# Kernel optimization log

Hardware: AMD Instinct MI355X
Metric: run time of the kernel (lower is better)

Reference implementation:

```python
import jax, jax.numpy as jnp
import numpy as np

SCALE = 0.1  # literal .mul(0.1) in the source, not 1/sqrt(d_k)


def setup_inputs() -> dict:
    key = jax.random.key(0)
    kq, kk, kv = jax.random.split(key, 3)
    B, S, D, Dv = 8, 2048, 1024, 1024
    q = jax.random.normal(kq, (B, S, D), dtype=jnp.float32)
    k = jax.random.normal(kk, (B, D, S), dtype=jnp.float32)  # note [B, D, S]: matmul(q, k) with no transpose
    v = jax.random.normal(kv, (B, S, Dv), dtype=jnp.float32)
    return {"q": q, "k": k, "v": v}


def reference(q, k, v):
    # s = (q @ k) * 0.1 ; a = softmax(s, -1) ; dropout in eval -> identity ; r = a @ v
    s = jnp.einsum('bsd,bdt->bst', q, k) * SCALE  # [B, S, S]
    a = jax.nn.softmax(s, axis=-1)
    r = jnp.einsum('bst,btv->bsv', a, v)          # [B, S, Dv]
    return r
```

## Files before the change

kernel.cpp:

```cpp
#include <hip/hip_runtime.h>
#include <stdint.h>

#define SEQ 2048
#define DHK 1024
#define DHV 1024
#define NB 8

typedef __attribute__((ext_vector_type(8))) short bf16x8;
typedef __attribute__((ext_vector_type(4))) float f32x4;

__device__ __forceinline__ unsigned short f2bf(float f) {
    uint32_t u = __builtin_bit_cast(uint32_t, f);
    u += 0x7fffu + ((u >> 16) & 1u);
    return (unsigned short)(u >> 16);
}

__device__ __forceinline__ void gload_lds16(const unsigned short* g, unsigned short* l) {
    __builtin_amdgcn_global_load_lds(
        (const __attribute__((address_space(1))) void*)g,
        (__attribute__((address_space(3))) void*)l,
        16, 0, 0);
}

#define WG_BARRIER() asm volatile("s_barrier" ::: "memory")

__global__ __launch_bounds__(256) void fused_cvt(const float* __restrict__ q,
                                                 const float* __restrict__ k,
                                                 const float* __restrict__ v,
                                                 unsigned short* __restrict__ Qb,
                                                 unsigned short* __restrict__ Kt,
                                                 unsigned short* __restrict__ Vt) {
    __shared__ float tile[64][65];
    int bid = blockIdx.x;
    if (bid < 4096) {
        size_t i = ((size_t)bid * 256 + threadIdx.x) * 16;
#pragma unroll
        for (int c = 0; c < 4; ++c) {
            float4 x = *(const float4*)(q + i + c * 4);
            ushort4 o;
            o.x = f2bf(x.x); o.y = f2bf(x.y); o.z = f2bf(x.z); o.w = f2bf(x.w);
            *(ushort4*)(Qb + i + c * 4) = o;
        }
        return;
    }
    const float* in;
    unsigned short* out;
    int R, C, b, x, y;
    if (bid < 8192) {
        int id = bid - 4096;
        b = id >> 9; int rem = id & 511;
        x = rem & 31; y = rem >> 5;
        in = k; out = Kt; R = DHK; C = SEQ;
    } else {
        int id = bid - 8192;
        b = id >> 9; int rem = id & 511;
        x = rem & 15; y = rem >> 4;
        in = v; out = Vt; R = SEQ; C = DHV;
    }
    int c0 = x * 64, r0 = y * 64;
    const float* ib = in + (size_t)b * R * C;
    unsigned short* ob = out + (size_t)b * R * C;
    int tr = threadIdx.x >> 4;
    int tc = (threadIdx.x & 15) * 4;
#pragma unroll
    for (int it = 0; it < 4; ++it) {
        int r = tr + it * 16;
        float4 w = *(const float4*)(ib + (size_t)(r0 + r) * C + c0 + tc);
        tile[r][tc + 0] = w.x; tile[r][tc + 1] = w.y;
        tile[r][tc + 2] = w.z; tile[r][tc + 3] = w.w;
    }
    __syncthreads();
#pragma unroll
    for (int it = 0; it < 4; ++it) {
        int c = tr + it * 16;
        ushort4 o;
        o.x = f2bf(tile[tc + 0][c]);
        o.y = f2bf(tile[tc + 1][c]);
        o.z = f2bf(tile[tc + 2][c]);
        o.w = f2bf(tile[tc + 3][c]);
        *(ushort4*)(ob + (size_t)(c0 + c) * R + r0 + tc) = o;
    }
}

template <int MODE>
__global__ __launch_bounds__(512, 2) void attn_gemm8(const unsigned short* __restrict__ A,
                                                     const unsigned short* __restrict__ Bt,
                                                     void* __restrict__ Cout) {
    constexpr int K   = (MODE == 0) ? DHK : SEQ;
    constexpr int N   = (MODE == 0) ? SEQ : DHV;
    constexpr int TN  = N / 256;
    constexpr int NKT = K / 64;
    constexpr int NITER = NKT / 2;

    __shared__ __attribute__((aligned(16))) unsigned short As[2][256 * 64];
    __shared__ __attribute__((aligned(16))) unsigned short Bs[2][256 * 64];

    const int lid   = blockIdx.x;
    const int batch = lid & 7;
    const int t     = lid >> 3;
    const int bm    = t / TN;
    const int bn    = t % TN;

    const int tid  = threadIdx.x;
    const int wv   = tid >> 6;
    const int lane = tid & 63;
    const int wm   = wv & 1;
    const int wn   = wv >> 1;
    const int m16  = lane & 15;
    const int q    = lane >> 4;
    const int sw   = m16 & 7;
    const int lane_row = lane >> 3;
    const int g    = (lane & 7) ^ lane_row;

    const unsigned short* Ab = A  + (size_t)batch * SEQ * K;
    const unsigned short* Bb = Bt + (size_t)batch * N * K;
    const unsigned short* Ag = Ab + (size_t)(bm * 256 + lane_row) * K + g * 8;
    const unsigned short* Bg = Bb + (size_t)(bn * 256 + lane_row) * K + g * 8;

    auto stage = [&](int ktile, int sub) {
        const int buf = ktile & 1;
        const int k0  = ktile * 64;
#pragma unroll
        for (int c = 0; c < 2; ++c) {
            const int lrow = wv * 16 + c * 8;
            if (sub < 2) {
                const int rb = sub * 128 + lrow;
                gload_lds16(Bg + (size_t)rb * K + k0, &Bs[buf][rb * 64]);
            } else {
                const int rb = (sub == 2 ? 0 : 64) + lrow + (lrow & 64);
                gload_lds16(Ag + (size_t)rb * K + k0, &As[buf][rb * 64]);
            }
        }
    };

    f32x4 acc[8][4];
#pragma unroll
    for (int i = 0; i < 8; ++i)
#pragma unroll
        for (int j = 0; j < 4; ++j)
#pragma unroll
            for (int e = 0; e < 4; ++e) acc[i][j][e] = 0.0f;

    f32x4 acc1[8];
#pragma unroll
    for (int i = 0; i < 8; ++i)
#pragma unroll
        for (int e = 0; e < 4; ++e) acc1[i][e] = 0.0f;
    const short one_bf = (short)0x3F80;
    const bf16x8 ones = {one_bf, one_bf, one_bf, one_bf, one_bf, one_bf, one_bf, one_bf};

#pragma unroll
    for (int ht = 0; ht < 7; ++ht) stage(ht >> 2, ht & 3);
    asm volatile("s_waitcnt vmcnt(6)" ::: "memory");
    WG_BARRIER();

    bf16x8 bfr[4][2];
#pragma unroll 1
    for (int it = 0; it < NITER; ++it) {
        const bool notlast = (it + 1 < NITER);
#pragma unroll
        for (int p = 0; p < 8; ++p) {
            const int qd   = p & 3;
            const int rbuf = p >> 2;
            bf16x8 af[2][2];
#pragma unroll
            for (int i = 0; i < 2; ++i) {
                const int mrow = wm * 128 + (qd * 2 + i) * 16 + m16;
#pragma unroll
                for (int ss = 0; ss < 2; ++ss)
                    af[i][ss] = *(const bf16x8*)&As[rbuf][mrow * 64 + ((ss * 4 + q) ^ sw) * 8];
            }
            if (qd == 0) {
#pragma unroll
                for (int nt = 0; nt < 4; ++nt) {
                    const int nrow = wn * 64 + nt * 16 + m16;
#pragma unroll
                    for (int ss = 0; ss < 2; ++ss)
                        bfr[nt][ss] = *(const bf16x8*)&Bs[rbuf][nrow * 64 + ((ss * 4 + q) ^ sw) * 8];
                }
            }
            if (p == 0 || notlast) stage((7 + it * 8 + p) >> 2, (7 + p) & 3);
            WG_BARRIER();
            __builtin_amdgcn_s_setprio(1);
#pragma unroll
            for (int ss = 0; ss < 2; ++ss)
#pragma unroll
                for (int i = 0; i < 2; ++i) {
                    const int mt = qd * 2 + i;
#pragma unroll
                    for (int nt = 0; nt < 4; ++nt)
                        acc[mt][nt] = __builtin_amdgcn_mfma_f32_16x16x32_bf16(
                            af[i][ss], bfr[nt][ss], acc[mt][nt], 0, 0, 0);
                    if (MODE == 1)
                        acc1[mt] = __builtin_amdgcn_mfma_f32_16x16x32_bf16(
                            af[i][ss], ones, acc1[mt], 0, 0, 0);
                }
            __builtin_amdgcn_s_setprio(0);
            if (qd == 3) {
                if (notlast) { asm volatile("s_waitcnt vmcnt(6)" ::: "memory"); }
                else         { asm volatile("s_waitcnt vmcnt(0)" ::: "memory"); }
            }
            WG_BARRIER();
        }
    }

    const int i0 = bm * 256 + wm * 128;
    const int t0 = bn * 256 + wn * 64;
    if (MODE == 0) {
        unsigned short* E = (unsigned short*)Cout + (size_t)batch * SEQ * N;
#pragma unroll
        for (int mt = 0; mt < 8; ++mt)
#pragma unroll
            for (int e = 0; e < 4; ++e) {
                int i = i0 + mt * 16 + q * 4 + e;
#pragma unroll
                for (int nt = 0; nt < 4; ++nt) {
                    int cc = t0 + nt * 16 + m16;
                    E[(size_t)i * N + cc] = f2bf(__expf(0.1f * acc[mt][nt][e]));
                }
            }
    } else {
        float* O = (float*)Cout + (size_t)batch * SEQ * N;
#pragma unroll
        for (int mt = 0; mt < 8; ++mt)
#pragma unroll
            for (int e = 0; e < 4; ++e) {
                int i = i0 + mt * 16 + q * 4 + e;
                float inv = 1.0f / acc1[mt][e];
#pragma unroll
                for (int nt = 0; nt < 4; ++nt) {
                    int cc = t0 + nt * 16 + m16;
                    O[(size_t)i * N + cc] = acc[mt][nt][e] * inv;
                }
            }
    }
}

extern "C" void kernel_launch(void* const* d_in, const int* in_sizes, int n_in,
                              void* d_out, int out_size, void* d_ws, size_t ws_size,
                              hipStream_t stream) {
    (void)in_sizes; (void)n_in; (void)out_size; (void)ws_size;
    const float* q = (const float*)d_in[0];
    const float* k = (const float*)d_in[1];
    const float* v = (const float*)d_in[2];

    char* ws = (char*)d_ws;
    unsigned short* Qb = (unsigned short*)(ws);
    unsigned short* Kt = (unsigned short*)(ws + 33554432);
    unsigned short* Vt = (unsigned short*)(ws + 67108864);
    unsigned short* E  = (unsigned short*)(ws + 100663296);

    fused_cvt<<<dim3(12288), dim3(256), 0, stream>>>(q, k, v, Qb, Kt, Vt);
    attn_gemm8<0><<<dim3(NB * 8 * 8), dim3(512), 0, stream>>>(Qb, Kt, (void*)E);
    attn_gemm8<1><<<dim3(NB * 8 * 4), dim3(512), 0, stream>>>(E, Vt, d_out);
}
```

Measured before the change: 369.9 us.

## Make QK GEMM persistent over two N tiles and compute row sums on VALU

The first GEMM now launches 256 workgroups, each computing two consecutive 256-wide N tiles. The global-to-LDS prefetch pipeline continues across the tile boundary instead of draining and refilling. The second GEMM drops the extra MFMA against a ones vector that computed softmax denominators. It accumulates row sums from the A fragments with scalar bf16-to-float adds plus cross-lane shuffles, which frees matrix-core issue slots but adds VALU work per step. The aim is to cut wave-quantization and pipeline-startup cost, at the price of fewer resident workgroups in the first GEMM.

```diff
diff --git a/kernel.cpp b/kernel.cpp
--- a/kernel.cpp
+++ b/kernel.cpp
@@ -13,6 +13,10 @@
     uint32_t u = __builtin_bit_cast(uint32_t, f);
     u += 0x7fffu + ((u >> 16) & 1u);
     return (unsigned short)(u >> 16);
+}
+
+__device__ __forceinline__ float bf2f(unsigned short s) {
+    return __builtin_bit_cast(float, (uint32_t)s << 16);
 }
 
 __device__ __forceinline__ void gload_lds16(const unsigned short* g, unsigned short* l) {
@@ -86,11 +90,13 @@
 __global__ __launch_bounds__(512, 2) void attn_gemm8(const unsigned short* __restrict__ A,
                                                      const unsigned short* __restrict__ Bt,
                                                      void* __restrict__ Cout) {
-    constexpr int K   = (MODE == 0) ? DHK : SEQ;
-    constexpr int N   = (MODE == 0) ? SEQ : DHV;
-    constexpr int TN  = N / 256;
-    constexpr int NKT = K / 64;
+    constexpr int K     = (MODE == 0) ? DHK : SEQ;
+    constexpr int N     = (MODE == 0) ? SEQ : DHV;
+    constexpr int REPS  = (MODE == 0) ? 2 : 1;
+    constexpr int NKT   = K / 64;
+    constexpr int LOGNKT = (MODE == 0) ? 4 : 5;
     constexpr int NITER = NKT / 2;
+    constexpr int TOTAL_HT = REPS * NKT * 4;
 
     __shared__ __attribute__((aligned(16))) unsigned short As[2][256 * 64];
     __shared__ __attribute__((aligned(16))) unsigned short Bs[2][256 * 64];
@@ -98,8 +104,8 @@
     const int lid   = blockIdx.x;
     const int batch = lid & 7;
     const int t     = lid >> 3;
-    const int bm    = t / TN;
-    const int bn    = t % TN;
+    const int bm    = t >> 2;
+    const int bn    = t & 3;
 
     const int tid  = threadIdx.x;
     const int wv   = tid >> 6;
@@ -115,17 +121,23 @@
     const unsigned short* Ab = A  + (size_t)batch * SEQ * K;
     const unsigned short* Bb = Bt + (size_t)batch * N * K;
     const unsigned short* Ag = Ab + (size_t)(bm * 256 + lane_row) * K + g * 8;
-    const unsigned short* Bg = Bb + (size_t)(bn * 256 + lane_row) * K + g * 8;
-
-    auto stage = [&](int ktile, int sub) {
-        const int buf = ktile & 1;
-        const int k0  = ktile * 64;
+    const unsigned short* Bg = Bb + (size_t)(bn * REPS * 256 + lane_row) * K + g * 8;
+
+    auto stage = [&](int ht) {
+        const int ktg = ht >> 2;
+        const int sub = ht & 3;
+        const int buf = ktg & 1;
+        int ktl, rps;
+        if constexpr (REPS > 1) { ktl = ktg & (NKT - 1); rps = ktg >> LOGNKT; }
+        else                    { ktl = ktg; rps = 0; }
+        const int k0 = ktl * 64;
+        const size_t brep = (size_t)rps * 256 * K;
 #pragma unroll
         for (int c = 0; c < 2; ++c) {
             const int lrow = wv * 16 + c * 8;
             if (sub < 2) {
                 const int rb = sub * 128 + lrow;
-                gload_lds16(Bg + (size_t)rb * K + k0, &Bs[buf][rb * 64]);
+                gload_lds16(Bg + brep + (size_t)rb * K + k0, &Bs[buf][rb * 64]);
             } else {
                 const int rb = (sub == 2 ? 0 : 64) + lrow + (lrow & 64);
                 gload_lds16(Ag + (size_t)rb * K + k0, &As[buf][rb * 64]);
@@ -134,105 +146,123 @@
     };
 
     f32x4 acc[8][4];
-#pragma unroll
-    for (int i = 0; i < 8; ++i)
-#pragma unroll
-        for (int j = 0; j < 4; ++j)
-#pragma unroll
-            for (int e = 0; e < 4; ++e) acc[i][j][e] = 0.0f;
-
-    f32x4 acc1[8];
-#pragma unroll
-    for (int i = 0; i < 8; ++i)
-#pragma unroll
-        for (int e = 0; e < 4; ++e) acc1[i][e] = 0.0f;
-    const short one_bf = (short)0x3F80;
-    const bf16x8 ones = {one_bf, one_bf, one_bf, one_bf, one_bf, one_bf, one_bf, one_bf};
-
-#pragma unroll
-    for (int ht = 0; ht < 7; ++ht) stage(ht >> 2, ht & 3);
+    float rs[8];
+#pragma unroll
+    for (int s = 0; s < 8; ++s) rs[s] = 0.0f;
+
+#pragma unroll
+    for (int ht = 0; ht < 7; ++ht) stage(ht);
     asm volatile("s_waitcnt vmcnt(6)" ::: "memory");
     WG_BARRIER();
 
     bf16x8 bfr[4][2];
 #pragma unroll 1
-    for (int it = 0; it < NITER; ++it) {
-        const bool notlast = (it + 1 < NITER);
-#pragma unroll
-        for (int p = 0; p < 8; ++p) {
-            const int qd   = p & 3;
-            const int rbuf = p >> 2;
-            bf16x8 af[2][2];
-#pragma unroll
-            for (int i = 0; i < 2; ++i) {
-                const int mrow = wm * 128 + (qd * 2 + i) * 16 + m16;
+    for (int rep = 0; rep < REPS; ++rep) {
+#pragma unroll
+        for (int i = 0; i < 8; ++i)
+#pragma unroll
+            for (int j = 0; j < 4; ++j)
+#pragma unroll
+                for (int e = 0; e < 4; ++e) acc[i][j][e] = 0.0f;
+
+#pragma unroll 1
+        for (int it = 0; it < NITER; ++it) {
+            const bool last_it = (rep == REPS - 1) && (it == NITER - 1);
+            const int ht_base = (rep * NITER + it) * 8 + 7;
+#pragma unroll
+            for (int p = 0; p < 8; ++p) {
+                const int qd   = p & 3;
+                const int rbuf = p >> 2;
+                bf16x8 af[2][2];
+#pragma unroll
+                for (int i = 0; i < 2; ++i) {
+                    const int mrow = wm * 128 + (qd * 2 + i) * 16 + m16;
+#pragma unroll
+                    for (int ss = 0; ss < 2; ++ss)
+                        af[i][ss] = *(const bf16x8*)&As[rbuf][mrow * 64 + ((ss * 4 + q) ^ sw) * 8];
+                }
+                if (qd == 0) {
+#pragma unroll
+                    for (int nt = 0; nt < 4; ++nt) {
+                        const int nrow = wn * 64 + nt * 16 + m16;
+#pragma unroll
+                        for (int ss = 0; ss < 2; ++ss)
+                            bfr[nt][ss] = *(const bf16x8*)&Bs[rbuf][nrow * 64 + ((ss * 4 + q) ^ sw) * 8];
+                    }
+                }
+                {
+                    const int ht = ht_base + p;
+                    if (ht < TOTAL_HT) stage(ht);
+                }
+                WG_BARRIER();
+                __builtin_amdgcn_s_setprio(1);
 #pragma unroll
                 for (int ss = 0; ss < 2; ++ss)
-                    af[i][ss] = *(const bf16x8*)&As[rbuf][mrow * 64 + ((ss * 4 + q) ^ sw) * 8];
+#pragma unroll
+                    for (int i = 0; i < 2; ++i) {
+                        const int mt = qd * 2 + i;
+#pragma unroll
+                        for (int nt = 0; nt < 4; ++nt)
+                            acc[mt][nt] = __builtin_amdgcn_mfma_f32_16x16x32_bf16(
+                                af[i][ss], bfr[nt][ss], acc[mt][nt], 0, 0, 0);
+                    }
+                __builtin_amdgcn_s_setprio(0);
+                if (MODE == 1) {
+#pragma unroll
+                    for (int i = 0; i < 2; ++i) {
+                        float s0 = 0.0f;
+#pragma unroll
+                        for (int ss = 0; ss < 2; ++ss)
+#pragma unroll
+                            for (int e = 0; e < 8; ++e)
+                                s0 += bf2f((unsigned short)af[i][ss][e]);
+                        rs[qd * 2 + i] += s0;
+                    }
+                }
+                if (qd == 3) {
+                    if (!last_it) { asm volatile("s_waitcnt vmcnt(6)" ::: "memory"); }
+                    else          { asm volatile("s_waitcnt vmcnt(0)" ::: "memory"); }
+                }
+                WG_BARRIER();
             }
-            if (qd == 0) {
-#pragma unroll
-                for (int nt = 0; nt < 4; ++nt) {
-                    const int nrow = wn * 64 + nt * 16 + m16;
-#pragma unroll
-                    for (int ss = 0; ss < 2; ++ss)
-                        bfr[nt][ss] = *(const bf16x8*)&Bs[rbuf][nrow * 64 + ((ss * 4 + q) ^ sw) * 8];
-                }
+        }
+
+        const int i0 = bm * 256 + wm * 128;
+        const int t0 = (bn * REPS + rep) * 256 + wn * 64;
+        if (MODE == 0) {
+            unsigned short* E = (unsigned short*)Cout + (size_t)batch * SEQ * N;
+#pragma unroll
+            for (int mt = 0; mt < 8; ++mt)
+#pragma unroll
+                for (int e = 0; e < 4; ++e) {
+                    int i = i0 + mt * 16 + q * 4 + e;
+#pragma unroll
+                    for (int nt = 0; nt < 4; ++nt) {
+                        int cc = t0 + nt * 16 + m16;
+                        E[(size_t)i * N + cc] = f2bf(__expf(0.1f * acc[mt][nt][e]));
+                    }
+                }
+        } else {
+#pragma unroll
+            for (int s = 0; s < 8; ++s) {
+                rs[s] += __shfl_xor(rs[s], 16);
+                rs[s] += __shfl_xor(rs[s], 32);
             }
-            if (p == 0 || notlast) stage((7 + it * 8 + p) >> 2, (7 + p) & 3);
-            WG_BARRIER();
-            __builtin_amdgcn_s_setprio(1);
-#pragma unroll
-            for (int ss = 0; ss < 2; ++ss)
-#pragma unroll
-                for (int i = 0; i < 2; ++i) {
-                    const int mt = qd * 2 + i;
-#pragma unroll
-                    for (int nt = 0; nt < 4; ++nt)
-                        acc[mt][nt] = __builtin_amdgcn_mfma_f32_16x16x32_bf16(
-                            af[i][ss], bfr[nt][ss], acc[mt][nt], 0, 0, 0);
-                    if (MODE == 1)
-                        acc1[mt] = __builtin_amdgcn_mfma_f32_16x16x32_bf16(
-                            af[i][ss], ones, acc1[mt], 0, 0, 0);
-                }
-            __builtin_amdgcn_s_setprio(0);
-            if (qd == 3) {
-                if (notlast) { asm volatile("s_waitcnt vmcnt(6)" ::: "memory"); }
-                else         { asm volatile("s_waitcnt vmcnt(0)" ::: "memory"); }
-            }
-            WG_BARRIER();
-        }
-    }
-
-    const int i0 = bm * 256 + wm * 128;
-    const int t0 = bn * 256 + wn * 64;
-    if (MODE == 0) {
-        unsigned short* E = (unsigned short*)Cout + (size_t)batch * SEQ * N;
-#pragma unroll
-        for (int mt = 0; mt < 8; ++mt)
-#pragma unroll
-            for (int e = 0; e < 4; ++e) {
-                int i = i0 + mt * 16 + q * 4 + e;
-#pragma unroll
-                for (int nt = 0; nt < 4; ++nt) {
-                    int cc = t0 + nt * 16 + m16;
-                    E[(size_t)i * N + cc] = f2bf(__expf(0.1f * acc[mt][nt][e]));
-                }
-            }
-    } else {
-        float* O = (float*)Cout + (size_t)batch * SEQ * N;
-#pragma unroll
-        for (int mt = 0; mt < 8; ++mt)
-#pragma unroll
-            for (int e = 0; e < 4; ++e) {
-                int i = i0 + mt * 16 + q * 4 + e;
-                float inv = 1.0f / acc1[mt][e];
-#pragma unroll
-                for (int nt = 0; nt < 4; ++nt) {
-                    int cc = t0 + nt * 16 + m16;
-                    O[(size_t)i * N + cc] = acc[mt][nt][e] * inv;
-                }
-            }
+            float* O = (float*)Cout + (size_t)batch * SEQ * N;
+#pragma unroll
+            for (int mt = 0; mt < 8; ++mt)
+#pragma unroll
+                for (int e = 0; e < 4; ++e) {
+                    int i = i0 + mt * 16 + q * 4 + e;
+                    float rsv = __shfl(rs[mt], q * 4 + e);
+                    float inv = 1.0f / rsv;
+#pragma unroll
+                    for (int nt = 0; nt < 4; ++nt) {
+                        int cc = t0 + nt * 16 + m16;
+                        O[(size_t)i * N + cc] = acc[mt][nt][e] * inv;
+                    }
+                }
+        }
     }
 }
 
@@ -251,6 +281,6 @@
     unsigned short* E  = (unsigned short*)(ws + 100663296);
 
     fused_cvt<<<dim3(12288), dim3(256), 0, stream>>>(q, k, v, Qb, Kt, Vt);
-    attn_gemm8<0><<<dim3(NB * 8 * 8), dim3(512), 0, stream>>>(Qb, Kt, (void*)E);
-    attn_gemm8<1><<<dim3(NB * 8 * 4), dim3(512), 0, stream>>>(E, Vt, d_out);
-}
+    attn_gemm8<0><<<dim3(256), dim3(512), 0, stream>>>(Qb, Kt, (void*)E);
+    attn_gemm8<1><<<dim3(256), dim3(512), 0, stream>>>(E, Vt, d_out);
+}
```

Result: slower. 649.4 us (+75.6%).
